# Performance work log

Hardware: AMD Instinct MI355X
Metric: run time of the kernel (lower is better)

## Reference

```python
import jax, jax.numpy as jnp
import numpy as np

D_MODEL = 512
N_HEADS = 8
D_Q = 64   # d_queries == d_keys
D_V = 64
LN_EPS = 1e-5


def setup_inputs() -> dict:
    key = jax.random.key(0)
    ks = jax.random.split(key, 10)
    N, S = 4, 2048
    x = jax.random.normal(ks[0], (N, S, D_MODEL), dtype=jnp.float32)
    lengths = jax.random.randint(ks[1], (N,), 1, S + 1)  # true lengths in [1, S]
    s = 0.02
    Wq = jax.random.normal(ks[2], (D_MODEL, N_HEADS * D_Q), dtype=jnp.float32) * s
    bq = jnp.zeros((N_HEADS * D_Q,), dtype=jnp.float32)
    Wkv = jax.random.normal(ks[3], (D_MODEL, N_HEADS * (D_Q + D_V)), dtype=jnp.float32) * s
    bkv = jnp.zeros((N_HEADS * (D_Q + D_V),), dtype=jnp.float32)
    Wo = jax.random.normal(ks[4], (N_HEADS * D_V, D_MODEL), dtype=jnp.float32) * s
    bo = jnp.zeros((D_MODEL,), dtype=jnp.float32)
    gamma = jnp.ones((D_MODEL,), dtype=jnp.float32)
    beta = jnp.zeros((D_MODEL,), dtype=jnp.float32)
    return {"x": x, "key_value_sequence_lengths": lengths, "Wq": Wq, "bq": bq,
            "Wkv": Wkv, "bkv": bkv, "Wo": Wo, "bo": bo, "gamma": gamma, "beta": beta}


def reference(x, key_value_sequence_lengths, Wq, bq, Wkv, bkv, Wo, bo, gamma, beta):
    # Decoder self-attention: query_sequences == key_value_sequences == x.
    N, S, _ = x.shape
    H, dq, dv = N_HEADS, D_Q, D_V

    residual = x
    # Pre-LayerNorm (applied to both queries and keys/values since self-attention)
    mu = jnp.mean(x, axis=-1, keepdims=True)
    var = jnp.var(x, axis=-1, keepdims=True)
    xn = (x - mu) * jax.lax.rsqrt(var + LN_EPS) * gamma + beta

    q = (xn @ Wq + bq).reshape(N, S, H, dq).transpose(0, 2, 1, 3)          # (N,H,S,dq)
    kv = xn @ Wkv + bkv
    k = kv[..., : H * dq].reshape(N, S, H, dq).transpose(0, 2, 1, 3)       # (N,H,S,dq)
    v = kv[..., H * dq :].reshape(N, S, H, dv).transpose(0, 2, 1, 3)       # (N,H,S,dv)

    scores = jnp.einsum("nhqd,nhkd->nhqk", q, k) / jnp.sqrt(jnp.float32(dq))  # (N,H,S,S)

    # Padding mask over keys + causal (not-future) mask
    key_pos = jnp.arange(S)
    pad_ok = key_pos[None, None, None, :] < key_value_sequence_lengths[:, None, None, None]
    causal_ok = (key_pos[None, :] <= jnp.arange(S)[:, None])[None, None, :, :]
    mask = pad_ok & causal_ok
    scores = jnp.where(mask, scores, -jnp.inf)

    attn = jax.nn.softmax(scores, axis=-1)
    out = jnp.einsum("nhqk,nhkd->nqhd", attn, v).reshape(N, S, H * dv)
    out = out @ Wo + bo
    return out + residual
```

## Files before the change

### kernel.cpp

```cpp
#include <hip/hip_runtime.h>
#include <hip/hip_bf16.h>

typedef __attribute__((ext_vector_type(4))) float f32x4;
typedef __attribute__((ext_vector_type(16))) float f32x16;
typedef __attribute__((ext_vector_type(8))) short short8;

#define D_MODEL 512
#define SQ 2048
#define NH 8
#define NBATCH 4
#define MROWS (NBATCH * SQ)

__device__ __forceinline__ ushort f2b(float x) {
  unsigned int u = __float_as_uint(x);
  return (ushort)((u + 0x7fffu + ((u >> 16) & 1u)) >> 16);
}

__device__ __forceinline__ f32x4 mfma16(short8 a, short8 b, f32x4 c) {
  return __builtin_amdgcn_mfma_f32_16x16x32_bf16(a, b, c, 0, 0, 0);
}
__device__ __forceinline__ f32x16 mfma32(short8 a, short8 b, f32x16 c) {
  return __builtin_amdgcn_mfma_f32_32x32x16_bf16(a, b, c, 0, 0, 0);
}

#define GLOAD_LDS16(g, l)                                                      \
  __builtin_amdgcn_global_load_lds(                                            \
      (const __attribute__((address_space(1))) unsigned int*)(g),              \
      (__attribute__((address_space(3))) unsigned int*)(l), 16, 0, 0)

__global__ __launch_bounds__(256) void transpose_w(const float* __restrict__ W,
                                                   ushort* __restrict__ WT,
                                                   int K, int N) {
  __shared__ ushort tile[32][33];
  int n0 = blockIdx.x * 32, k0 = blockIdx.y * 32;
  int tx = threadIdx.x & 31, ty = threadIdx.x >> 5;
#pragma unroll
  for (int i = 0; i < 4; ++i) {
    int k = ty + i * 8;
    tile[tx][k] = f2b(W[(size_t)(k0 + k) * N + n0 + tx]);
  }
  __syncthreads();
#pragma unroll
  for (int i = 0; i < 4; ++i) {
    int nn = ty + i * 8;
    WT[(size_t)(n0 + nn) * K + k0 + tx] = tile[nn][tx];
  }
}

__global__ __launch_bounds__(256) void ln_kernel(const float* __restrict__ x,
                                                 const float* __restrict__ gamma,
                                                 const float* __restrict__ beta,
                                                 ushort* __restrict__ xn) {
  int wid = threadIdx.x >> 6, lane = threadIdx.x & 63;
  int row = blockIdx.x * 4 + wid;
  const float4* xr = (const float4*)(x + (size_t)row * D_MODEL);
  float4 v0 = xr[lane];
  float4 v1 = xr[lane + 64];
  float s = v0.x + v0.y + v0.z + v0.w + v1.x + v1.y + v1.z + v1.w;
  float q = v0.x * v0.x + v0.y * v0.y + v0.z * v0.z + v0.w * v0.w +
            v1.x * v1.x + v1.y * v1.y + v1.z * v1.z + v1.w * v1.w;
#pragma unroll
  for (int m = 1; m < 64; m <<= 1) {
    s += __shfl_xor(s, m, 64);
    q += __shfl_xor(q, m, 64);
  }
  float mu = s * (1.f / 512.f);
  float var = q * (1.f / 512.f) - mu * mu;
  float rs = rsqrtf(var + 1e-5f);
  const float4* g4 = (const float4*)gamma;
  const float4* b4 = (const float4*)beta;
  ushort* out = xn + (size_t)row * D_MODEL;
#pragma unroll
  for (int i = 0; i < 2; ++i) {
    float4 v = i ? v1 : v0;
    float4 gg = g4[lane + i * 64];
    float4 bb = b4[lane + i * 64];
    ushort4 o;
    o.x = f2b((v.x - mu) * rs * gg.x + bb.x);
    o.y = f2b((v.y - mu) * rs * gg.y + bb.y);
    o.z = f2b((v.z - mu) * rs * gg.z + bb.z);
    o.w = f2b((v.w - mu) * rs * gg.w + bb.w);
    *(ushort4*)(out + (lane + i * 64) * 4) = o;
  }
}

__global__ __launch_bounds__(256) void qkv_gemm(
    const ushort* __restrict__ A, const ushort* __restrict__ BT,
    const float* __restrict__ bq, const float* __restrict__ bkv,
    ushort* __restrict__ qbuf, ushort* __restrict__ kvbuf, float qscale) {
  __shared__ __align__(16) ushort As[128 * 32];
  __shared__ __align__(16) ushort Bs[128 * 32];
  const int tid = threadIdx.x, lane = tid & 63, wid = tid >> 6;
  const int g = lane >> 4, r = lane & 15;
  const int wr = wid >> 1, wc = wid & 1;
  const int bm = blockIdx.y * 128, bn = blockIdx.x * 128;

  f32x4 acc[4][4];
#pragma unroll
  for (int a = 0; a < 4; ++a)
#pragma unroll
    for (int b = 0; b < 4; ++b) acc[a][b] = (f32x4){0.f, 0.f, 0.f, 0.f};

  const int srow = 32 * wid + (lane >> 2);
  const int scol = (lane & 3) * 8;
  const ushort* ga = A + (size_t)(bm + srow) * 512 + scol;
  const ushort* gb = BT + (size_t)(bn + srow) * 512 + scol;
  ushort* la = As + 32 * 32 * wid;
  ushort* lb = Bs + 32 * 32 * wid;

  for (int kb = 0; kb < 512; kb += 32) {
    __syncthreads();
    GLOAD_LDS16(ga + kb, la);
    GLOAD_LDS16(ga + kb + 16 * 512, la + 16 * 32);
    GLOAD_LDS16(gb + kb, lb);
    GLOAD_LDS16(gb + kb + 16 * 512, lb + 16 * 32);
    __syncthreads();
    short8 af[4], bf[4];
#pragma unroll
    for (int i2 = 0; i2 < 4; ++i2) {
      af[i2] = *(const short8*)&As[(wr * 64 + i2 * 16 + r) * 32 + g * 8];
      bf[i2] = *(const short8*)&Bs[(wc * 64 + i2 * 16 + r) * 32 + g * 8];
    }
#pragma unroll
    for (int a = 0; a < 4; ++a)
#pragma unroll
      for (int b = 0; b < 4; ++b) acc[a][b] = mfma16(af[a], bf[b], acc[a][b]);
  }

  const bool isQ = (bn < 512);
  const float* bias = isQ ? bq : bkv;
  ushort* dst = isQ ? qbuf : kvbuf;
  const int cb = isQ ? bn : bn - 512;
  const size_t stride = isQ ? 512 : 1024;
  const float scale = isQ ? qscale : 1.0f;

#pragma unroll
  for (int a = 0; a < 4; ++a) {
#pragma unroll
    for (int reg = 0; reg < 4; ++reg) {
      int row = bm + wr * 64 + a * 16 + g * 4 + reg;
#pragma unroll
      for (int b = 0; b < 4; ++b) {
        int col = cb + wc * 64 + b * 16 + r;
        dst[(size_t)row * stride + col] = f2b((acc[a][b][reg] + bias[col]) * scale);
      }
    }
  }
}

__global__ __launch_bounds__(256) void o_gemm(
    const ushort* __restrict__ A, const ushort* __restrict__ BT,
    const float* __restrict__ bias, const float* __restrict__ resid,
    float* __restrict__ outF) {
  __shared__ __align__(16) ushort As[128 * 32];
  __shared__ __align__(16) ushort Bs[128 * 32];
  const int tid = threadIdx.x, lane = tid & 63, wid = tid >> 6;
  const int g = lane >> 4, r = lane & 15;
  const int wr = wid >> 1, wc = wid & 1;
  const int bm = blockIdx.y * 128, bn = blockIdx.x * 128;

  f32x4 acc[4][4];
#pragma unroll
  for (int a = 0; a < 4; ++a)
#pragma unroll
    for (int b = 0; b < 4; ++b) acc[a][b] = (f32x4){0.f, 0.f, 0.f, 0.f};

  const int srow = 32 * wid + (lane >> 2);
  const int scol = (lane & 3) * 8;
  const ushort* ga = A + (size_t)(bm + srow) * 512 + scol;
  const ushort* gb = BT + (size_t)(bn + srow) * 512 + scol;
  ushort* la = As + 32 * 32 * wid;
  ushort* lb = Bs + 32 * 32 * wid;

  for (int kb = 0; kb < 512; kb += 32) {
    __syncthreads();
    GLOAD_LDS16(ga + kb, la);
    GLOAD_LDS16(ga + kb + 16 * 512, la + 16 * 32);
    GLOAD_LDS16(gb + kb, lb);
    GLOAD_LDS16(gb + kb + 16 * 512, lb + 16 * 32);
    __syncthreads();
    short8 af[4], bf[4];
#pragma unroll
    for (int i2 = 0; i2 < 4; ++i2) {
      af[i2] = *(const short8*)&As[(wr * 64 + i2 * 16 + r) * 32 + g * 8];
      bf[i2] = *(const short8*)&Bs[(wc * 64 + i2 * 16 + r) * 32 + g * 8];
    }
#pragma unroll
    for (int a = 0; a < 4; ++a)
#pragma unroll
      for (int b = 0; b < 4; ++b) acc[a][b] = mfma16(af[a], bf[b], acc[a][b]);
  }

#pragma unroll
  for (int a = 0; a < 4; ++a) {
#pragma unroll
    for (int reg = 0; reg < 4; ++reg) {
      int row = bm + wr * 64 + a * 16 + g * 4 + reg;
#pragma unroll
      for (int b = 0; b < 4; ++b) {
        int col = bn + wc * 64 + b * 16 + r;
        outF[(size_t)row * 512 + col] =
            acc[a][b][reg] + bias[col] + resid[(size_t)row * 512 + col];
      }
    }
  }
}

__global__ __launch_bounds__(256) void attn_kernel(
    const ushort* __restrict__ qbuf, const ushort* __restrict__ kvbuf,
    const int* __restrict__ lengths, ushort* __restrict__ partialO,
    float2* __restrict__ mlbuf) {
  __shared__ __align__(16) ushort smem[9728];

  const int tid = threadIdx.x, lane = tid & 63, wid = tid >> 6;
  const int l31 = lane & 31, h = lane >> 5;

  const int bx = blockIdx.x;
  const int nh = bx / 40;
  const int L = bx - nh * 40;
  const int n = nh >> 3, head = nh & 7;
  int qi, c;
  if (L < 4) { qi = L; c = 0; }
  else if (L < 12) { qi = 4 + ((L - 4) >> 1); c = (L - 4) & 1; }
  else if (L < 24) { qi = 8 + (L - 12) / 3; c = (L - 12) % 3; }
  else { qi = 12 + ((L - 24) >> 2); c = (L - 24) & 3; }
  const int slot = bx;

  const int qb = qi * 128;
  const int len = lengths[n];
  const int q0w = qb + 32 * wid;
  const int q_own = q0w + l31;
  const int nt_w_abs = 4 * qi + wid + 1;
  const int t0 = c * 16;
  const int t1 = min(t0 + 16, 4 * qi + 4);
  const int tlen = (len + 31) >> 5;
  int nt = min(t1, tlen) - t0;
  if (nt < 0) nt = 0;

  short8 qf[4];
  {
    const ushort* qp = qbuf + (size_t)(n * SQ + q_own) * 512 + head * 64 + 8 * h;
#pragma unroll
    for (int kc = 0; kc < 4; ++kc) qf[kc] = *(const short8*)(qp + 16 * kc);
  }

  f32x16 o0, o1;
#pragma unroll
  for (int i = 0; i < 16; ++i) { o0[i] = 0.f; o1[i] = 0.f; }
  float m_ = -1e30f, ls = 0.f;

  const int skey = tid >> 3, sc8 = tid & 7;
  const int kp = lane & 15, dvb = wid * 4 + (lane >> 4);
  const int mu = (l31 >> 2) & 3;

  int voff[4];
#pragma unroll
  for (int j = 0; j < 4; ++j) {
    int dv = 4 * dvb + j;
    voff[j] = dv * 20 + (((kp >> 2) ^ ((dv >> 2) & 3)) << 2) + (kp & 3);
  }

  const ushort* kvbase = kvbuf + (size_t)n * SQ * 1024 + head * 64;
  const ushort* kSrc = kvbase + (size_t)(t0 * 32 + skey) * 1024 + sc8 * 8;
  const ushort* vSrc = kvbase + 512 + (size_t)(t0 * 32 + 2 * kp) * 1024 + dvb * 4;
  const int kLdsOff = skey * 72 + sc8 * 8;

  if (nt > 0) {
    uint4 kreg;
    uint2 va, vb;
    kreg = *(const uint4*)kSrc;
    va = *(const uint2*)vSrc;
    vb = *(const uint2*)(vSrc + 1024);
    kSrc += 32 * 1024;
    vSrc += 32 * 1024;
    {
      *(uint4*)(smem + kLdsOff) = kreg;
      const ushort* a16 = (const ushort*)&va;
      const ushort* b16 = (const ushort*)&vb;
#pragma unroll
      for (int j = 0; j < 4; ++j)
        ((unsigned*)(smem + 4608))[voff[j]] =
            (unsigned)a16[j] | ((unsigned)b16[j] << 16);
    }
    __syncthreads();

    for (int i = 0; i < nt; ++i) {
      const int t = t0 + i;
      const int cur = i & 1;
      const bool more = (i + 1 < nt);
      uint4 kreg2;
      uint2 va2, vb2;
      if (more) {
        kreg2 = *(const uint4*)kSrc;
        va2 = *(const uint2*)vSrc;
        vb2 = *(const uint2*)(vSrc + 1024);
        kSrc += 32 * 1024;
        vSrc += 32 * 1024;
      }

      if (t < nt_w_abs) {
        const int kb = t * 32;
        const ushort* KtB = smem + cur * 2304;
        const ushort* VtB = smem + 4608 + cur * 2560;

        f32x16 s;
#pragma unroll
        for (int i2 = 0; i2 < 16; ++i2) s[i2] = 0.f;
        {
          const ushort* kr_ = KtB + l31 * 72 + 8 * h;
          short8 k0 = *(const short8*)(kr_);
          short8 k1 = *(const short8*)(kr_ + 16);
          short8 k2 = *(const short8*)(kr_ + 32);
          short8 k3 = *(const short8*)(kr_ + 48);
          s = mfma32(k0, qf[0], s);
          s = mfma32(k1, qf[1], s);
          s = mfma32(k2, qf[2], s);
          s = mfma32(k3, qf[3], s);
        }

        if (kb + 31 > q0w || kb + 31 >= len) {
          int keyb = kb + 4 * h;
#pragma unroll
          for (int reg = 0; reg < 16; ++reg) {
            int key = keyb + (reg & 3) + 8 * (reg >> 2);
            bool ok = (key <= q_own) && (key < len);
            s[reg] = ok ? s[reg] : -1e30f;
          }
        }

        float mx = s[0];
#pragma unroll
        for (int reg = 1; reg < 16; ++reg) mx = fmaxf(mx, s[reg]);
        {
          auto rr = __builtin_amdgcn_permlane32_swap(__float_as_uint(mx),
                                                     __float_as_uint(mx), false, false);
          mx = fmaxf(__uint_as_float(((const unsigned*)&rr)[0]),
                     __uint_as_float(((const unsigned*)&rr)[1]));
        }

        if (!__all(mx <= m_ + 8.0f)) {
          float mn = fmaxf(m_, mx);
          float sf = __builtin_amdgcn_exp2f(m_ - mn);
          m_ = mn;
          ls *= sf;
#pragma unroll
          for (int i2 = 0; i2 < 16; ++i2) { o0[i2] *= sf; o1[i2] *= sf; }
        }

        float p[16];
#pragma unroll
        for (int reg = 0; reg < 16; ++reg)
          p[reg] = __builtin_amdgcn_exp2f(s[reg] - m_);

        float rsum = ((p[0] + p[1]) + (p[2] + p[3])) + ((p[4] + p[5]) + (p[6] + p[7])) +
                     ((p[8] + p[9]) + (p[10] + p[11])) +
                     ((p[12] + p[13]) + (p[14] + p[15]));
        {
          auto rr = __builtin_amdgcn_permlane32_swap(__float_as_uint(rsum),
                                                     __float_as_uint(rsum), false, false);
          rsum = __uint_as_float(((const unsigned*)&rr)[0]) +
                 __uint_as_float(((const unsigned*)&rr)[1]);
        }
        ls += rsum;

        unsigned pk[8];
#pragma unroll
        for (int j = 0; j < 8; ++j)
          pk[j] = __builtin_amdgcn_perm(__float_as_uint(p[2 * j + 1]),
                                        __float_as_uint(p[2 * j]), 0x07060302u);

#pragma unroll
        for (int kc = 0; kc < 2; ++kc) {
          short8 pf;
          ((unsigned*)&pf)[0] = pk[4 * kc + 0];
          ((unsigned*)&pf)[1] = pk[4 * kc + 1];
          ((unsigned*)&pf)[2] = pk[4 * kc + 2];
          ((unsigned*)&pf)[3] = pk[4 * kc + 3];
          const int u0 = ((2 * kc) ^ mu) << 3;
          const ushort* vb0 = VtB + l31 * 40 + 4 * h;
          const ushort* vb1 = VtB + (32 + l31) * 40 + 4 * h;
          short8 vf0, vf1;
          ((uint2*)&vf0)[0] = *(const uint2*)(vb0 + u0);
          ((uint2*)&vf0)[1] = *(const uint2*)(vb0 + (u0 ^ 8));
          ((uint2*)&vf1)[0] = *(const uint2*)(vb1 + u0);
          ((uint2*)&vf1)[1] = *(const uint2*)(vb1 + (u0 ^ 8));
          o0 = mfma32(vf0, pf, o0);
          o1 = mfma32(vf1, pf, o1);
        }
      }

      if (more) {
        ushort* KtN = smem + (cur ^ 1) * 2304;
        unsigned* VtN = (unsigned*)(smem + 4608 + (cur ^ 1) * 2560);
        *(uint4*)(KtN + kLdsOff) = kreg2;
        const ushort* a16 = (const ushort*)&va2;
        const ushort* b16 = (const ushort*)&vb2;
#pragma unroll
        for (int j = 0; j < 4; ++j)
          VtN[voff[j]] = (unsigned)a16[j] | ((unsigned)b16[j] << 16);
      }
      __syncthreads();
    }
  }

  {
    float inv = (ls > 0.f) ? 1.f / ls : 0.f;
    ushort* OtW = smem + wid * (32 * 68);
#pragma unroll
    for (int b = 0; b < 2; ++b) {
#pragma unroll
      for (int reg = 0; reg < 16; reg += 2) {
        float e0 = (b ? o1[reg] : o0[reg]) * inv;
        float e1 = (b ? o1[reg + 1] : o0[reg + 1]) * inv;
        unsigned pko = __builtin_amdgcn_perm(__float_as_uint(e1),
                                             __float_as_uint(e0), 0x07060302u);
        int dv = 32 * b + (reg & 3) + 8 * (reg >> 2) + 4 * h;
        *(unsigned*)(OtW + l31 * 68 + dv) = pko;
      }
    }
    if (h == 0) mlbuf[slot * 128 + 32 * wid + l31] = make_float2(m_, ls);
  }
  __syncthreads();
  {
    int r = lane >> 1, sg = lane & 1;
    const ushort* rp = smem + wid * (32 * 68) + r * 68 + sg * 32;
    uint2 d0 = *(const uint2*)(rp);
    uint2 d1 = *(const uint2*)(rp + 4);
    uint2 d2 = *(const uint2*)(rp + 8);
    uint2 d3 = *(const uint2*)(rp + 12);
    uint2 d4 = *(const uint2*)(rp + 16);
    uint2 d5 = *(const uint2*)(rp + 20);
    uint2 d6 = *(const uint2*)(rp + 24);
    uint2 d7 = *(const uint2*)(rp + 28);
    ushort* gp = partialO + (size_t)slot * 8192 + (32 * wid + r) * 64 + sg * 32;
    *(uint4*)(gp) = make_uint4(d0.x, d0.y, d1.x, d1.y);
    *(uint4*)(gp + 8) = make_uint4(d2.x, d2.y, d3.x, d3.y);
    *(uint4*)(gp + 16) = make_uint4(d4.x, d4.y, d5.x, d5.y);
    *(uint4*)(gp + 24) = make_uint4(d6.x, d6.y, d7.x, d7.y);
  }
}

__global__ __launch_bounds__(256) void attn_combine(
    const ushort* __restrict__ partialO, const float2* __restrict__ mlbuf,
    ushort* __restrict__ attout) {
  const int bx = blockIdx.x;
  const int nh = bx >> 4, qi = bx & 15;
  const int n = nh >> 3, head = nh & 7;
  int off, nch;
  if (qi < 4) { off = qi; nch = 1; }
  else if (qi < 8) { off = 4 + 2 * (qi - 4); nch = 2; }
  else if (qi < 12) { off = 12 + 3 * (qi - 8); nch = 3; }
  else { off = 24 + 4 * (qi - 12); nch = 4; }
  const int slot0 = nh * 40 + off;

  const int tid = threadIdx.x;
  const int r = tid >> 1, half = tid & 1;

  float2 ml[4];
  float mstar = -1e30f;
#pragma unroll
  for (int c = 0; c < 4; ++c)
    if (c < nch) {
      ml[c] = mlbuf[(slot0 + c) * 128 + r];
      mstar = fmaxf(mstar, ml[c].x);
    }
  float coef[4];
  float Lsum = 0.f;
#pragma unroll
  for (int c = 0; c < 4; ++c)
    if (c < nch) {
      coef[c] = (ml[c].y > 0.f)
                    ? ml[c].y * __builtin_amdgcn_exp2f(ml[c].x - mstar)
                    : 0.f;
      Lsum += coef[c];
    }

  float acc[32];
#pragma unroll
  for (int j = 0; j < 32; ++j) acc[j] = 0.f;

#pragma unroll
  for (int c = 0; c < 4; ++c)
    if (c < nch) {
      const float cf = coef[c];
      const uint4* p =
          (const uint4*)(partialO + (size_t)(slot0 + c) * 8192 + r * 64 + half * 32);
#pragma unroll
      for (int u = 0; u < 4; ++u) {
        uint4 d = p[u];
        unsigned w[4] = {d.x, d.y, d.z, d.w};
#pragma unroll
        for (int k = 0; k < 4; ++k) {
          acc[u * 8 + 2 * k] += cf * __uint_as_float(w[k] << 16);
          acc[u * 8 + 2 * k + 1] += cf * __uint_as_float(w[k] & 0xffff0000u);
        }
      }
    }

  const float inv = 1.f / Lsum;
  uint4 outw[4];
#pragma unroll
  for (int u = 0; u < 4; ++u) {
    unsigned ww[4];
#pragma unroll
    for (int k = 0; k < 4; ++k) {
      float e0 = acc[u * 8 + 2 * k] * inv;
      float e1 = acc[u * 8 + 2 * k + 1] * inv;
      ww[k] = ((unsigned)f2b(e0)) | (((unsigned)f2b(e1)) << 16);
    }
    outw[u] = make_uint4(ww[0], ww[1], ww[2], ww[3]);
  }
  ushort* gp = attout + (size_t)(n * SQ + qi * 128 + r) * 512 + head * 64 + half * 32;
#pragma unroll
  for (int u = 0; u < 4; ++u) ((uint4*)gp)[u] = outw[u];
}

extern "C" void kernel_launch(void* const* d_in, const int* in_sizes, int n_in,
                              void* d_out, int out_size, void* d_ws, size_t ws_size,
                              hipStream_t stream) {
  const float* x = (const float*)d_in[0];
  const int* lens = (const int*)d_in[1];
  const float* Wq = (const float*)d_in[2];
  const float* bq = (const float*)d_in[3];
  const float* Wkv = (const float*)d_in[4];
  const float* bkv = (const float*)d_in[5];
  const float* Wo = (const float*)d_in[6];
  const float* bo = (const float*)d_in[7];
  const float* gamma = (const float*)d_in[8];
  const float* beta = (const float*)d_in[9];
  float* out = (float*)d_out;

  size_t off = 0;
  auto alloc = [&](size_t bytes) {
    void* p = (char*)d_ws + off;
    off += (bytes + 255) & ~(size_t)255;
    return p;
  };
  ushort* xn = (ushort*)alloc((size_t)MROWS * 512 * 2);
  ushort* qbuf = (ushort*)alloc((size_t)MROWS * 512 * 2);
  ushort* kvbuf = (ushort*)alloc((size_t)MROWS * 1024 * 2);
  ushort* WT = (ushort*)alloc((size_t)1536 * 512 * 2);
  ushort* WoT = (ushort*)alloc((size_t)512 * 512 * 2);
  ushort* partialO = (ushort*)alloc((size_t)1280 * 8192 * 2);
  float2* mlbuf = (float2*)alloc((size_t)1280 * 128 * 8);
  ushort* attout = xn;

  transpose_w<<<dim3(16, 16), 256, 0, stream>>>(Wq, WT, 512, 512);
  transpose_w<<<dim3(32, 16), 256, 0, stream>>>(Wkv, WT + 512 * 512, 512, 1024);
  transpose_w<<<dim3(16, 16), 256, 0, stream>>>(Wo, WoT, 512, 512);

  ln_kernel<<<MROWS / 4, 256, 0, stream>>>(x, gamma, beta, xn);

  qkv_gemm<<<dim3(12, 64), 256, 0, stream>>>(xn, WT, bq, bkv, qbuf, kvbuf,
                                             0.125f * 1.44269504f);

  attn_kernel<<<dim3(1280), 256, 0, stream>>>(qbuf, kvbuf, lens, partialO, mlbuf);
  attn_combine<<<dim3(512), 256, 0, stream>>>(partialO, mlbuf, attout);

  o_gemm<<<dim3(4, 64), 256, 0, stream>>>(attout, WoT, bo, x, out);
}
```

Baseline: 123.9 us.

## Split attention key ranges into finer balanced chunks and skip dead partial writes

Changes the split-K work decomposition of the causal attention kernel. The old scheme used 40 chunks of up to 16 key tiles per batch-head; the new one uses 72 chunks, with roughly (qi+2)/2 chunks per query block and keys divided evenly among them. The goal is more blocks and shorter, more even per-block work across the GPU. It also skips partial-output stores for rows whose softmax sum is zero, and the combine kernel skips reading chunks whose coefficient is zero. The cost is more partial slots for the combine pass to read and merge.

```diff
diff --git a/kernel.cpp b/kernel.cpp
--- a/kernel.cpp
+++ b/kernel.cpp
@@ -10,6 +10,9 @@
 #define NH 8
 #define NBATCH 4
 #define MROWS (NBATCH * SQ)
+
+#define CHUNKS_PER_NH 72
+#define NSLOTS (32 * CHUNKS_PER_NH)
 
 __device__ __forceinline__ ushort f2b(float x) {
   unsigned int u = __float_as_uint(x);
@@ -216,14 +219,14 @@
   const int l31 = lane & 31, h = lane >> 5;
 
   const int bx = blockIdx.x;
-  const int nh = bx / 40;
-  const int L = bx - nh * 40;
+  const int nh = bx / CHUNKS_PER_NH;
+  const int L = bx - nh * CHUNKS_PER_NH;
   const int n = nh >> 3, head = nh & 7;
-  int qi, c;
-  if (L < 4) { qi = L; c = 0; }
-  else if (L < 12) { qi = 4 + ((L - 4) >> 1); c = (L - 4) & 1; }
-  else if (L < 24) { qi = 8 + (L - 12) / 3; c = (L - 12) % 3; }
-  else { qi = 12 + ((L - 24) >> 2); c = (L - 24) & 3; }
+  int qi = 0, c = L;
+  while (c >= ((qi + 2) >> 1)) { c -= (qi + 2) >> 1; ++qi; }
+  const int T = 4 * qi + 4, nch = (qi + 2) >> 1;
+  const int t0 = (c * T) / nch;
+  const int t1 = ((c + 1) * T) / nch;
   const int slot = bx;
 
   const int qb = qi * 128;
@@ -231,8 +234,6 @@
   const int q0w = qb + 32 * wid;
   const int q_own = q0w + l31;
   const int nt_w_abs = 4 * qi + wid + 1;
-  const int t0 = c * 16;
-  const int t1 = min(t0 + 16, 4 * qi + 4);
   const int tlen = (len + 31) >> 5;
   int nt = min(t1, tlen) - t0;
   if (nt < 0) nt = 0;
@@ -403,6 +404,7 @@
     }
   }
 
+  const unsigned long long alive = __ballot(ls > 0.f);
   {
     float inv = (ls > 0.f) ? 1.f / ls : 0.f;
     ushort* OtW = smem + wid * (32 * 68);
@@ -421,22 +423,24 @@
     if (h == 0) mlbuf[slot * 128 + 32 * wid + l31] = make_float2(m_, ls);
   }
   __syncthreads();
-  {
+  if (alive) {
     int r = lane >> 1, sg = lane & 1;
-    const ushort* rp = smem + wid * (32 * 68) + r * 68 + sg * 32;
-    uint2 d0 = *(const uint2*)(rp);
-    uint2 d1 = *(const uint2*)(rp + 4);
-    uint2 d2 = *(const uint2*)(rp + 8);
-    uint2 d3 = *(const uint2*)(rp + 12);
-    uint2 d4 = *(const uint2*)(rp + 16);
-    uint2 d5 = *(const uint2*)(rp + 20);
-    uint2 d6 = *(const uint2*)(rp + 24);
-    uint2 d7 = *(const uint2*)(rp + 28);
-    ushort* gp = partialO + (size_t)slot * 8192 + (32 * wid + r) * 64 + sg * 32;
-    *(uint4*)(gp) = make_uint4(d0.x, d0.y, d1.x, d1.y);
-    *(uint4*)(gp + 8) = make_uint4(d2.x, d2.y, d3.x, d3.y);
-    *(uint4*)(gp + 16) = make_uint4(d4.x, d4.y, d5.x, d5.y);
-    *(uint4*)(gp + 24) = make_uint4(d6.x, d6.y, d7.x, d7.y);
+    if ((alive >> r) & 1ULL) {
+      const ushort* rp = smem + wid * (32 * 68) + r * 68 + sg * 32;
+      uint2 d0 = *(const uint2*)(rp);
+      uint2 d1 = *(const uint2*)(rp + 4);
+      uint2 d2 = *(const uint2*)(rp + 8);
+      uint2 d3 = *(const uint2*)(rp + 12);
+      uint2 d4 = *(const uint2*)(rp + 16);
+      uint2 d5 = *(const uint2*)(rp + 20);
+      uint2 d6 = *(const uint2*)(rp + 24);
+      uint2 d7 = *(const uint2*)(rp + 28);
+      ushort* gp = partialO + (size_t)slot * 8192 + (32 * wid + r) * 64 + sg * 32;
+      *(uint4*)(gp) = make_uint4(d0.x, d0.y, d1.x, d1.y);
+      *(uint4*)(gp + 8) = make_uint4(d2.x, d2.y, d3.x, d3.y);
+      *(uint4*)(gp + 16) = make_uint4(d4.x, d4.y, d5.x, d5.y);
+      *(uint4*)(gp + 24) = make_uint4(d6.x, d6.y, d7.x, d7.y);
+    }
   }
 }
 
@@ -445,43 +449,44 @@
     ushort* __restrict__ attout) {
   const int bx = blockIdx.x;
   const int nh = bx >> 4, qi = bx & 15;
+  int off = 0;
+#pragma unroll
+  for (int j = 0; j < 15; ++j) off += (j < qi) ? ((j + 2) >> 1) : 0;
+  const int nch = (qi + 2) >> 1;
   const int n = nh >> 3, head = nh & 7;
-  int off, nch;
-  if (qi < 4) { off = qi; nch = 1; }
-  else if (qi < 8) { off = 4 + 2 * (qi - 4); nch = 2; }
-  else if (qi < 12) { off = 12 + 3 * (qi - 8); nch = 3; }
-  else { off = 24 + 4 * (qi - 12); nch = 4; }
-  const int slot0 = nh * 40 + off;
+  const int slot0 = nh * CHUNKS_PER_NH + off;
 
   const int tid = threadIdx.x;
   const int r = tid >> 1, half = tid & 1;
 
-  float2 ml[4];
+  float2 ml[8];
   float mstar = -1e30f;
 #pragma unroll
-  for (int c = 0; c < 4; ++c)
+  for (int c = 0; c < 8; ++c)
     if (c < nch) {
       ml[c] = mlbuf[(slot0 + c) * 128 + r];
       mstar = fmaxf(mstar, ml[c].x);
     }
-  float coef[4];
+  float coef[8];
   float Lsum = 0.f;
 #pragma unroll
-  for (int c = 0; c < 4; ++c)
+  for (int c = 0; c < 8; ++c) {
+    coef[c] = 0.f;
     if (c < nch) {
       coef[c] = (ml[c].y > 0.f)
                     ? ml[c].y * __builtin_amdgcn_exp2f(ml[c].x - mstar)
                     : 0.f;
       Lsum += coef[c];
     }
+  }
 
   float acc[32];
 #pragma unroll
   for (int j = 0; j < 32; ++j) acc[j] = 0.f;
 
 #pragma unroll
-  for (int c = 0; c < 4; ++c)
-    if (c < nch) {
+  for (int c = 0; c < 8; ++c)
+    if (c < nch && coef[c] != 0.f) {
       const float cf = coef[c];
       const uint4* p =
           (const uint4*)(partialO + (size_t)(slot0 + c) * 8192 + r * 64 + half * 32);
@@ -541,8 +546,8 @@
   ushort* kvbuf = (ushort*)alloc((size_t)MROWS * 1024 * 2);
   ushort* WT = (ushort*)alloc((size_t)1536 * 512 * 2);
   ushort* WoT = (ushort*)alloc((size_t)512 * 512 * 2);
-  ushort* partialO = (ushort*)alloc((size_t)1280 * 8192 * 2);
-  float2* mlbuf = (float2*)alloc((size_t)1280 * 128 * 8);
+  ushort* partialO = (ushort*)alloc((size_t)NSLOTS * 8192 * 2);
+  float2* mlbuf = (float2*)alloc((size_t)NSLOTS * 128 * 8);
   ushort* attout = xn;
 
   transpose_w<<<dim3(16, 16), 256, 0, stream>>>(Wq, WT, 512, 512);
@@ -554,7 +559,7 @@
   qkv_gemm<<<dim3(12, 64), 256, 0, stream>>>(xn, WT, bq, bkv, qbuf, kvbuf,
                                              0.125f * 1.44269504f);
 
-  attn_kernel<<<dim3(1280), 256, 0, stream>>>(qbuf, kvbuf, lens, partialO, mlbuf);
+  attn_kernel<<<dim3(NSLOTS), 256, 0, stream>>>(qbuf, kvbuf, lens, partialO, mlbuf);
   attn_combine<<<dim3(512), 256, 0, stream>>>(partialO, mlbuf, attout);
 
   o_gemm<<<dim3(4, 64), 256, 0, stream>>>(attout, WoT, bo, x, out);
```

After: 122.3 us. No clear change (-1.3%).
